# Kernel optimization log

Hardware: AMD Instinct MI355X
Metric: run time of the kernel (lower is better)

The kernel has to match this reference:

```python
import jax, jax.numpy as jnp
import numpy as np

BLOCK = 128
QMAX = 127.0


def act_quant(x2d):
    # Per (row, 128-wide block) symmetric int8 quantization.
    # x2d: [M, K] -> q int8-valued [M, K], scales [M, K//BLOCK]
    M, K = x2d.shape
    xb = x2d.reshape(M, K // BLOCK, BLOCK)
    s = jnp.max(jnp.abs(xb), axis=-1) / QMAX            # [M, K//BLOCK]
    s = jnp.maximum(s, 1e-12)
    q = jnp.clip(jnp.round(xb / s[..., None]), -128.0, 127.0)
    return q, s  # q kept in fp32 (exact small ints)


def weight_quant(w):
    # w: [N, K] -> q [N, K], scales [N//BLOCK, K//BLOCK]
    N, K = w.shape
    wb = w.reshape(N // BLOCK, BLOCK, K // BLOCK, BLOCK)
    s = jnp.max(jnp.abs(wb), axis=(1, 3)) / QMAX        # [N//BLOCK, K//BLOCK]
    s = jnp.maximum(s, 1e-12)
    q = jnp.clip(jnp.round(wb / s[:, None, :, None]), -128.0, 127.0)
    return q.reshape(N, K), s


def setup_inputs() -> dict:
    key = jax.random.key(0)
    k1, k2, k3 = jax.random.split(key, 3)
    x = jax.random.normal(k1, (4, 2048, 4096), dtype=jnp.float32)
    weight = jax.random.normal(k2, (4096, 4096), dtype=jnp.float32) * 0.02
    bias = jax.random.normal(k3, (4096,), dtype=jnp.float32) * 0.02
    return {"x": x, "weight": weight, "bias": bias}


def reference(x, weight, bias):
    # Int8Linear.forward: block-quantize activation, int8 GEMM with
    # grouped dequant scales (equivalent to dequantize-then-matmul), add bias.
    orig_shape = x.shape
    K = weight.shape[1]
    N = weight.shape[0]
    x2d = x.reshape(-1, K)                              # [M, K]
    M = x2d.shape[0]

    xq, xs = act_quant(x2d)                             # [M,Kb,128], [M,Kb]
    wq, ws = weight_quant(weight)                       # [N,K],     [Nb,Kb]

    # Dequantize (exact factorization of the scaled int8 GEMM):
    # out[m,n] = sum_kb xs[m,kb]*ws[nb,kb] * sum_c xq[m,kb,c]*wq[n,kb,c]
    x_dq = (xq * xs[..., None]).reshape(M, K)
    wqb = wq.reshape(N // BLOCK, BLOCK, K // BLOCK, BLOCK)
    w_dq = (wqb * ws[:, None, :, None]).reshape(N, K)

    out = x_dq @ w_dq.T + bias                          # [M, N]
    return out.reshape(orig_shape[:-1] + (N,))
```

## Files before the change

kernel.cpp:

```cpp
#include <hip/hip_runtime.h>
#include <stdint.h>

#define K_DIM 4096
#define N_DIM 4096
#define KB    32
#define QMAXF 127.0f

typedef int v4i __attribute__((ext_vector_type(4)));

__device__ __forceinline__ void async_copy16(void* lds, const void* gptr) {
    __builtin_amdgcn_global_load_lds(
        (__attribute__((address_space(1))) void*)gptr,
        (__attribute__((address_space(3))) void*)lds, 16, 0, 0);
}

__global__ __launch_bounds__(256) void act_quant_kernel(
    const float* __restrict__ x, int8_t* __restrict__ xq,
    float* __restrict__ xs_t, int M)
{
    const int t = threadIdx.x;
    for (int m = blockIdx.x; m < M; m += gridDim.x) {
        const float* xrow = x + (size_t)m * K_DIM;
        int8_t* qrow = xq + (size_t)m * K_DIM;

#pragma unroll
        for (int p = 0; p < 4; ++p) {
            const int base = p * 1024 + t * 4;
            float4 v = *(const float4*)(xrow + base);
            float a = fmaxf(fmaxf(fabsf(v.x), fabsf(v.y)), fmaxf(fabsf(v.z), fabsf(v.w)));
#pragma unroll
            for (int off = 1; off < 32; off <<= 1)
                a = fmaxf(a, __shfl_xor(a, off, 64));
            const float s = fmaxf(a / QMAXF, 1e-12f);
            const float inv = 1.0f / s;
            float q0 = fminf(fmaxf(rintf(v.x * inv), -128.f), 127.f);
            float q1 = fminf(fmaxf(rintf(v.y * inv), -128.f), 127.f);
            float q2 = fminf(fmaxf(rintf(v.z * inv), -128.f), 127.f);
            float q3 = fminf(fmaxf(rintf(v.w * inv), -128.f), 127.f);
            char4 pk;
            pk.x = (char)(int)q0; pk.y = (char)(int)q1;
            pk.z = (char)(int)q2; pk.w = (char)(int)q3;
            *(char4*)(qrow + base) = pk;
            if ((t & 31) == 0) {
                const int g = base >> 7;
                xs_t[(size_t)g * M + m] = s;
            }
        }
    }
}

__global__ __launch_bounds__(256) void weight_quant_kernel(
    const float* __restrict__ w, int8_t* __restrict__ wq, float* __restrict__ ws)
{
    const int nb = blockIdx.x >> 5;
    const int kb = blockIdx.x & 31;
    const int t  = threadIdx.x;
    const int n0 = nb * 128, k0 = kb * 128;

    float4 vals[16];
    float a = 0.f;
#pragma unroll
    for (int ii = 0; ii < 16; ++ii) {
        const int e = ii * 1024 + t * 4;
        const int row = e >> 7, col = e & 127;
        float4 v = *(const float4*)(w + (size_t)(n0 + row) * K_DIM + k0 + col);
        vals[ii] = v;
        a = fmaxf(a, fmaxf(fmaxf(fabsf(v.x), fabsf(v.y)), fmaxf(fabsf(v.z), fabsf(v.w))));
    }
#pragma unroll
    for (int off = 1; off < 64; off <<= 1)
        a = fmaxf(a, __shfl_xor(a, off, 64));
    __shared__ float wred[4];
    if ((t & 63) == 0) wred[t >> 6] = a;
    __syncthreads();
    a = fmaxf(fmaxf(wred[0], wred[1]), fmaxf(wred[2], wred[3]));
    const float s = fmaxf(a / QMAXF, 1e-12f);
    const float inv = 1.0f / s;
    if (t == 0) ws[nb * KB + kb] = s;

#pragma unroll
    for (int ii = 0; ii < 16; ++ii) {
        const int e = ii * 1024 + t * 4;
        const int row = e >> 7, col = e & 127;
        float4 v = vals[ii];
        char4 pk;
        pk.x = (char)(int)fminf(fmaxf(rintf(v.x * inv), -128.f), 127.f);
        pk.y = (char)(int)fminf(fmaxf(rintf(v.y * inv), -128.f), 127.f);
        pk.z = (char)(int)fminf(fmaxf(rintf(v.z * inv), -128.f), 127.f);
        pk.w = (char)(int)fminf(fmaxf(rintf(v.w * inv), -128.f), 127.f);
        *(char4*)(wq + (size_t)(n0 + row) * K_DIM + k0 + col) = pk;
    }
}

__global__ __launch_bounds__(256, 2) void gemm_kernel(
    const int8_t* __restrict__ xq, const int8_t* __restrict__ wq,
    const float* __restrict__ xs_t, const float* __restrict__ ws,
    const float* __restrict__ bias, float* __restrict__ out, int M)
{
    __shared__ __align__(16) int8_t As[2][128 * 128];
    __shared__ __align__(16) int8_t Bs[2][128 * 128];
    __shared__ __align__(16) float  xs_lds[2][128];

    const int t    = threadIdx.x;
    const int lane = t & 63;
    const int wave = t >> 6;

    const int nwg  = gridDim.x;
    const int cpx  = nwg >> 3;
    const int bid  = blockIdx.x;
    const int tile = (bid & 7) * cpx + (bid >> 3);
    const int nbt  = tile & 31;
    const int mbt  = tile >> 5;
    const int n0   = nbt * 128;
    const int m0   = mbt * 128;

    const int wm    = (wave >> 1) * 64;
    const int wn    = (wave & 1) * 64;
    const int frow  = lane & 15;
    const int q     = lane >> 4;
    const int quad4 = q * 4;
    const int sw0   = (q ^ (frow & 7)) * 16;
    const int wsrow = nbt * KB;

    int st_off[4];
#pragma unroll
    for (int it = 0; it < 4; ++it) {
        const int ci  = it * 256 + t;
        const int row = ci >> 3;
        const int c   = (ci & 7) ^ (row & 7);
        st_off[it] = row * K_DIM + c * 16;
    }

    const int8_t* Abase = xq + (size_t)m0 * K_DIM;
    const int8_t* Bbase = wq + (size_t)n0 * K_DIM;

    float4 facc[4][4] = {};

#pragma unroll
    for (int it = 0; it < 4; ++it) {
        async_copy16(&As[0][(it * 256 + wave * 64) * 16], Abase + st_off[it]);
        async_copy16(&Bs[0][(it * 256 + wave * 64) * 16], Bbase + st_off[it]);
    }
    if (t < 32)
        async_copy16(&xs_lds[0][0], xs_t + m0 + t * 4);
    __syncthreads();

    for (int kb = 0; kb < KB; ++kb) {
        const int cur = kb & 1;
        const int nxt = cur ^ 1;

        if (kb + 1 < KB) {
            const int8_t* Agn = Abase + (size_t)(kb + 1) * 128;
            const int8_t* Bgn = Bbase + (size_t)(kb + 1) * 128;
#pragma unroll
            for (int it = 0; it < 4; ++it) {
                async_copy16(&As[nxt][(it * 256 + wave * 64) * 16], Agn + st_off[it]);
                async_copy16(&Bs[nxt][(it * 256 + wave * 64) * 16], Bgn + st_off[it]);
            }
            if (t < 32)
                async_copy16(&xs_lds[nxt][0], xs_t + (size_t)(kb + 1) * M + m0 + t * 4);
        }

        const float wskb = ws[wsrow + kb];

        v4i a0[4], a1[4], b0[4], b1[4];
        float4 xs4[4];
#pragma unroll
        for (int i = 0; i < 4; ++i) {
            const int r = (wm + i * 16 + frow) * 128;
            a0[i] = *(const v4i*)&As[cur][r + sw0];
            a1[i] = *(const v4i*)&As[cur][r + (sw0 ^ 64)];
        }
#pragma unroll
        for (int j = 0; j < 4; ++j) {
            const int r = (wn + j * 16 + frow) * 128;
            b0[j] = *(const v4i*)&Bs[cur][r + sw0];
            b1[j] = *(const v4i*)&Bs[cur][r + (sw0 ^ 64)];
        }
#pragma unroll
        for (int i = 0; i < 4; ++i)
            xs4[i] = *(const float4*)&xs_lds[cur][wm + i * 16 + quad4];

#pragma unroll
        for (int i = 0; i < 4; ++i) {
            const float s0 = xs4[i].x * wskb, s1 = xs4[i].y * wskb;
            const float s2 = xs4[i].z * wskb, s3 = xs4[i].w * wskb;
#pragma unroll
            for (int j = 0; j < 4; ++j) {
                v4i d = __builtin_amdgcn_mfma_i32_16x16x64_i8(a0[i], b0[j], (v4i){0, 0, 0, 0}, 0, 0, 0);
                d = __builtin_amdgcn_mfma_i32_16x16x64_i8(a1[i], b1[j], d, 0, 0, 0);
                facc[i][j].x += (float)d[0] * s0;
                facc[i][j].y += (float)d[1] * s1;
                facc[i][j].z += (float)d[2] * s2;
                facc[i][j].w += (float)d[3] * s3;
            }
        }

        __syncthreads();
    }

    float bj[4];
#pragma unroll
    for (int j = 0; j < 4; ++j) bj[j] = bias[n0 + wn + j * 16 + frow];
#pragma unroll
    for (int i = 0; i < 4; ++i) {
#pragma unroll
        for (int r = 0; r < 4; ++r) {
            const int row = m0 + wm + i * 16 + quad4 + r;
            float* orow = out + (size_t)row * N_DIM + n0 + wn + frow;
#pragma unroll
            for (int j = 0; j < 4; ++j)
                orow[j * 16] = ((const float*)&facc[i][j])[r] + bj[j];
        }
    }
}

extern "C" void kernel_launch(void* const* d_in, const int* in_sizes, int n_in,
                              void* d_out, int out_size, void* d_ws, size_t ws_size,
                              hipStream_t stream)
{
    const float* x    = (const float*)d_in[0];
    const float* w    = (const float*)d_in[1];
    const float* bias = (const float*)d_in[2];
    float* out = (float*)d_out;
    const int M = in_sizes[0] / K_DIM;

    int8_t* xq  = (int8_t*)d_ws;
    int8_t* wqp = xq + (size_t)M * K_DIM;
    float*  xst = (float*)(wqp + (size_t)N_DIM * K_DIM);
    float*  wsp = xst + (size_t)KB * M;

    act_quant_kernel<<<2048, 256, 0, stream>>>(x, xq, xst, M);
    weight_quant_kernel<<<(N_DIM / 128) * KB, 256, 0, stream>>>(w, wqp, wsp);
    gemm_kernel<<<(N_DIM / 128) * (M / 128), 256, 0, stream>>>(
        xq, wqp, xst, wsp, bias, out, M);
}
```

Before: 474.9 us.

## Halve GEMM K-tile to 64 and raise occupancy to four workgroups per CU

The int8 GEMM now stages 64-wide K slices in LDS instead of 128-wide, halving shared memory per workgroup. Launch bounds are raised to allow four workgroups per CU, and the LDS swizzle is changed to fit 64-byte rows. The XCD-aware tile remapping is replaced by a plain 2D grid. The per-64 int32 MFMA result is converted to float and scaled twice as often, and dropping the remap may reduce L2 reuse across XCDs.

Result: slower. 498.3 us (+4.9%).

```diff
diff --git a/kernel.cpp b/kernel.cpp
--- a/kernel.cpp
+++ b/kernel.cpp
@@ -92,43 +92,39 @@
     }
 }
 
-__global__ __launch_bounds__(256, 2) void gemm_kernel(
+__global__ __launch_bounds__(256, 4) void gemm_kernel(
     const int8_t* __restrict__ xq, const int8_t* __restrict__ wq,
     const float* __restrict__ xs_t, const float* __restrict__ ws,
     const float* __restrict__ bias, float* __restrict__ out, int M)
 {
-    __shared__ __align__(16) int8_t As[2][128 * 128];
-    __shared__ __align__(16) int8_t Bs[2][128 * 128];
+    __shared__ __align__(16) int8_t As[2][128 * 64];
+    __shared__ __align__(16) int8_t Bs[2][128 * 64];
     __shared__ __align__(16) float  xs_lds[2][128];
 
     const int t    = threadIdx.x;
     const int lane = t & 63;
     const int wave = t >> 6;
 
-    const int nwg  = gridDim.x;
-    const int cpx  = nwg >> 3;
-    const int bid  = blockIdx.x;
-    const int tile = (bid & 7) * cpx + (bid >> 3);
-    const int nbt  = tile & 31;
-    const int mbt  = tile >> 5;
-    const int n0   = nbt * 128;
-    const int m0   = mbt * 128;
+    const int nbt = blockIdx.x;
+    const int mbt = blockIdx.y;
+    const int n0  = nbt * 128;
+    const int m0  = mbt * 128;
 
     const int wm    = (wave >> 1) * 64;
     const int wn    = (wave & 1) * 64;
     const int frow  = lane & 15;
     const int q     = lane >> 4;
     const int quad4 = q * 4;
-    const int sw0   = (q ^ (frow & 7)) * 16;
+    const int sw0   = ((q ^ frow ^ (frow >> 2)) & 3) * 16;
     const int wsrow = nbt * KB;
 
-    int st_off[4];
-#pragma unroll
-    for (int it = 0; it < 4; ++it) {
-        const int ci  = it * 256 + t;
-        const int row = ci >> 3;
-        const int c   = (ci & 7) ^ (row & 7);
-        st_off[it] = row * K_DIM + c * 16;
+    int st_off[2];
+#pragma unroll
+    for (int it = 0; it < 2; ++it) {
+        const int slot = it * 256 + t;
+        const int r    = slot >> 2;
+        const int c    = ((slot & 3) ^ r ^ (r >> 2)) & 3;
+        st_off[it] = r * K_DIM + c * 16;
     }
 
     const int8_t* Abase = xq + (size_t)m0 * K_DIM;
@@ -137,7 +133,7 @@
     float4 facc[4][4] = {};
 
 #pragma unroll
-    for (int it = 0; it < 4; ++it) {
+    for (int it = 0; it < 2; ++it) {
         async_copy16(&As[0][(it * 256 + wave * 64) * 16], Abase + st_off[it]);
         async_copy16(&Bs[0][(it * 256 + wave * 64) * 16], Bbase + st_off[it]);
     }
@@ -145,50 +141,41 @@
         async_copy16(&xs_lds[0][0], xs_t + m0 + t * 4);
     __syncthreads();
 
-    for (int kb = 0; kb < KB; ++kb) {
-        const int cur = kb & 1;
+    for (int s = 0; s < 2 * KB; ++s) {
+        const int cur = s & 1;
         const int nxt = cur ^ 1;
-
-        if (kb + 1 < KB) {
-            const int8_t* Agn = Abase + (size_t)(kb + 1) * 128;
-            const int8_t* Bgn = Bbase + (size_t)(kb + 1) * 128;
-#pragma unroll
-            for (int it = 0; it < 4; ++it) {
-                async_copy16(&As[nxt][(it * 256 + wave * 64) * 16], Agn + st_off[it]);
-                async_copy16(&Bs[nxt][(it * 256 + wave * 64) * 16], Bgn + st_off[it]);
+        const int kb  = s >> 1;
+
+        if (s + 1 < 2 * KB) {
+            const size_t kcol = (size_t)(s + 1) * 64;
+#pragma unroll
+            for (int it = 0; it < 2; ++it) {
+                async_copy16(&As[nxt][(it * 256 + wave * 64) * 16], Abase + kcol + st_off[it]);
+                async_copy16(&Bs[nxt][(it * 256 + wave * 64) * 16], Bbase + kcol + st_off[it]);
             }
-            if (t < 32)
-                async_copy16(&xs_lds[nxt][0], xs_t + (size_t)(kb + 1) * M + m0 + t * 4);
+            if ((s & 1) == 0 && t < 32)
+                async_copy16(&xs_lds[(kb + 1) & 1][0],
+                             xs_t + (size_t)(kb + 1) * M + m0 + t * 4);
         }
 
         const float wskb = ws[wsrow + kb];
 
-        v4i a0[4], a1[4], b0[4], b1[4];
-        float4 xs4[4];
+        v4i a[4], b[4];
+#pragma unroll
+        for (int i = 0; i < 4; ++i)
+            a[i] = *(const v4i*)&As[cur][(wm + i * 16 + frow) * 64 + sw0];
+#pragma unroll
+        for (int j = 0; j < 4; ++j)
+            b[j] = *(const v4i*)&Bs[cur][(wn + j * 16 + frow) * 64 + sw0];
+
 #pragma unroll
         for (int i = 0; i < 4; ++i) {
-            const int r = (wm + i * 16 + frow) * 128;
-            a0[i] = *(const v4i*)&As[cur][r + sw0];
-            a1[i] = *(const v4i*)&As[cur][r + (sw0 ^ 64)];
-        }
-#pragma unroll
-        for (int j = 0; j < 4; ++j) {
-            const int r = (wn + j * 16 + frow) * 128;
-            b0[j] = *(const v4i*)&Bs[cur][r + sw0];
-            b1[j] = *(const v4i*)&Bs[cur][r + (sw0 ^ 64)];
-        }
-#pragma unroll
-        for (int i = 0; i < 4; ++i)
-            xs4[i] = *(const float4*)&xs_lds[cur][wm + i * 16 + quad4];
-
-#pragma unroll
-        for (int i = 0; i < 4; ++i) {
-            const float s0 = xs4[i].x * wskb, s1 = xs4[i].y * wskb;
-            const float s2 = xs4[i].z * wskb, s3 = xs4[i].w * wskb;
+            const float4 xs4 = *(const float4*)&xs_lds[kb & 1][wm + i * 16 + quad4];
+            const float s0 = xs4.x * wskb, s1 = xs4.y * wskb;
+            const float s2 = xs4.z * wskb, s3 = xs4.w * wskb;
 #pragma unroll
             for (int j = 0; j < 4; ++j) {
-                v4i d = __builtin_amdgcn_mfma_i32_16x16x64_i8(a0[i], b0[j], (v4i){0, 0, 0, 0}, 0, 0, 0);
-                d = __builtin_amdgcn_mfma_i32_16x16x64_i8(a1[i], b1[j], d, 0, 0, 0);
+                v4i d = __builtin_amdgcn_mfma_i32_16x16x64_i8(a[i], b[j], (v4i){0, 0, 0, 0}, 0, 0, 0);
                 facc[i][j].x += (float)d[0] * s0;
                 facc[i][j].y += (float)d[1] * s1;
                 facc[i][j].z += (float)d[2] * s2;
@@ -232,6 +219,6 @@
 
     act_quant_kernel<<<2048, 256, 0, stream>>>(x, xq, xst, M);
     weight_quant_kernel<<<(N_DIM / 128) * KB, 256, 0, stream>>>(w, wqp, wsp);
-    gemm_kernel<<<(N_DIM / 128) * (M / 128), 256, 0, stream>>>(
+    gemm_kernel<<<dim3(N_DIM / 128, M / 128), 256, 0, stream>>>(
         xq, wqp, xst, wsp, bias, out, M);
 }
```
